# Kernel optimization log

Hardware: AMD Instinct MI355X
Metric: run time of the kernel (lower is better)

The kernel has to match this reference:

```python
import jax, jax.numpy as jnp
from jax import lax
import numpy as np

# Hyperparameters (module defaults)
MIP_K = 31
P_LO, P_HI = 0.01, 0.99
ALPHA = 0.15
MU = 10.0
PD_ITERS = 30
TAU = 0.125
SIG_PD = 0.125
THETA = 1.0
EPS = 1e-6


def _forward_grad(u):
    # forward differences, zero-padded on the far edge -> same shape as u
    dx = jnp.pad(u[..., :, 1:] - u[..., :, :-1], ((0, 0), (0, 0), (0, 0), (0, 1)))
    dy = jnp.pad(u[..., 1:, :] - u[..., :-1, :], ((0, 0), (0, 0), (0, 1), (0, 0)))
    return dx, dy


def _divergence(px, py):
    # backward-difference divergence (adjoint of forward grad)
    div_x = px - jnp.pad(px[..., :, :-1], ((0, 0), (0, 0), (0, 0), (1, 0)))
    div_y = py - jnp.pad(py[..., :-1, :], ((0, 0), (0, 0), (1, 0), (0, 0)))
    return div_x + div_y


def _max_pool(x, k):
    # stride-1 max pool with -inf padding (matches torch F.max_pool2d semantics)
    pad = k // 2
    return lax.reduce_window(
        x, -jnp.inf, lax.max,
        window_dimensions=(1, 1, k, k),
        window_strides=(1, 1, 1, 1),
        padding=((0, 0), (0, 0), (pad, pad), (pad, pad)))


def setup_inputs() -> dict:
    key = jax.random.key(0)
    Iy = jax.random.uniform(key, (16, 3, 512, 512), dtype=jnp.float32)
    return {"Iy": Iy}


def reference(Iy):
    R, G, Bc = Iy[:, 0:1], Iy[:, 1:2], Iy[:, 2:3]

    # MIP coarse depth
    Rmax = _max_pool(R, MIP_K)
    GBmax = jnp.maximum(_max_pool(G, MIP_K), _max_pool(Bc, MIP_K))
    x = jnp.abs(Rmax - GBmax) + R

    # robust per-image percentile normalization to [0,1]
    B = x.shape[0]
    flat = x.reshape(B, -1)
    lo = jnp.quantile(flat, P_LO, axis=1)[:, None, None, None]
    hi = jnp.quantile(flat, P_HI, axis=1)[:, None, None, None]
    N_hat = jnp.clip((x - lo) / (hi - lo + EPS), 0.0, 1.0)

    # fixed edge weights from grad(N_hat), sigma = per-image median grad magnitude
    dxh, dyh = _forward_grad(N_hat)
    grad_mag = jnp.sqrt(dxh * dxh + dyh * dyh + EPS)
    sigma = jnp.maximum(
        jnp.quantile(grad_mag.reshape(B, -1), 0.5, axis=1), EPS)[:, None, None, None]
    Wx = 1.0 + MU * jnp.exp(-jnp.abs(dxh) / sigma)
    Wy = 1.0 + MU * jnp.exp(-jnp.abs(dyh) / sigma)

    # Chambolle-Pock primal-dual iterations for weighted TV-L2
    def step(carry, _):
        u, u_bar, px, py = carry
        dx, dy = _forward_grad(u_bar)
        px = jnp.clip(px + SIG_PD * dx, -ALPHA * Wx, ALPHA * Wx)
        py = jnp.clip(py + SIG_PD * dy, -ALPHA * Wy, ALPHA * Wy)
        v = u + TAU * _divergence(px, py)
        u_new = (v + TAU * N_hat) / (1.0 + TAU)
        u_bar = u_new + THETA * (u_new - u)
        return (u_new, u_bar, px, py), None

    z = jnp.zeros_like(N_hat)
    (u, _, _, _), _ = lax.scan(step, (N_hat, N_hat, z, z), None, length=PD_ITERS)
    return jnp.clip(u, 0.0, 1.0)
```

## Files before the change

kernel.cpp:

```cpp
#include <hip/hip_runtime.h>
#include <math.h>

#define B_ 16
#define W_ 512
#define H_ 512
#define S_ (W_*H_)
#define ALPHA_ 0.15f
#define MU_ 10.0f
#define TAU_ 0.125f
#define SIG_ 0.125f
#define EPS_ 1e-6f
#define INV1PT_ (1.0f/(1.0f+TAU_))
#define NBINS 4096
#define BINSCALE 2048.0f
#define BINW (1.0f/2048.0f)

__global__ __launch_bounds__(256) void hmax_kernel(const float* __restrict__ Iy,
                                                   float* __restrict__ Rh,
                                                   float* __restrict__ GBh){
  __shared__ float bufA[2][544], bufB[2][544];
  int t = threadIdx.x;
  int b = blockIdx.x >> 9;
  int i = blockIdx.x & 511;
  const float* rowR = Iy + (size_t)b*3*S_ + (size_t)i*W_;
  const float* rowG = rowR + S_;
  const float* rowB = rowR + 2*S_;
  if (t < 128){
    int o4 = (t + 4)*4;
    float4 r = *(const float4*)&rowR[o4-16];
    float4 g = *(const float4*)&rowG[o4-16];
    float4 bb = *(const float4*)&rowB[o4-16];
    *(float4*)&bufA[0][o4] = r;
    *(float4*)&bufA[1][o4] = make_float4(fmaxf(g.x,bb.x), fmaxf(g.y,bb.y),
                                         fmaxf(g.z,bb.z), fmaxf(g.w,bb.w));
  } else if (t < 160){
    int e = t - 128;
    int p = (e < 16) ? e : (512 + e);
    bufA[0][p] = -1e30f;
    bufA[1][p] = -1e30f;
  }
  __syncthreads();
  float (*src)[544] = bufA; float (*dst)[544] = bufB;
  const int ds[5] = {1, 2, 4, 8, 15};
  #pragma unroll
  for (int sstep = 0; sstep < 5; ++sstep){
    int d = ds[sstep];
    for (int p = t; p < 544; p += 256){
      int q = min(p + d, 543);
      dst[0][p] = fmaxf(src[0][p], src[0][q]);
      dst[1][p] = fmaxf(src[1][p], src[1][q]);
    }
    __syncthreads();
    float (*tmp)[544] = src; src = dst; dst = tmp;
  }
  size_t o = (size_t)b*S_ + (size_t)i*W_;
  for (int p = t; p < 512; p += 256){
    Rh[o+p]  = src[0][p+1];
    GBh[o+p] = src[1][p+1];
  }
}

__global__ __launch_bounds__(256) void vscan_fwd_kernel(const float* __restrict__ Rh,
                                                        const float* __restrict__ GBh,
                                                        float* __restrict__ Rf,
                                                        float* __restrict__ Gf){
  int gid = blockIdx.x*256 + threadIdx.x;
  int col = gid & 8191;
  int c   = gid >> 13;
  int b = col >> 9, j = col & 511;
  int i0 = c*31;
  size_t base = (size_t)b*S_ + j;
  float rR = -1e30f, rG = -1e30f;
  if (c <= 15){
    for (int k = 0; k < 31; ++k){
      size_t o = base + (size_t)(i0+k)*W_;
      rR = fmaxf(rR, Rh[o]); rG = fmaxf(rG, GBh[o]);
      Rf[o] = rR; Gf[o] = rG;
    }
  } else {
    for (int k = 0; k < 16; ++k){
      size_t o = base + (size_t)(i0+k)*W_;
      rR = fmaxf(rR, Rh[o]); rG = fmaxf(rG, GBh[o]);
      Rf[o] = rR; Gf[o] = rG;
    }
  }
}

__global__ __launch_bounds__(256) void vscan_bwd_kernel(const float* __restrict__ Rh,
                                                        const float* __restrict__ GBh,
                                                        const float* __restrict__ Rf,
                                                        const float* __restrict__ Gf,
                                                        const float* __restrict__ Iy,
                                                        float* __restrict__ xo,
                                                        unsigned int* __restrict__ hist){
  __shared__ unsigned int h[NBINS];
  int t = threadIdx.x;
  for (int p = t; p < NBINS; p += 256) h[p] = 0u;
  __syncthreads();
  int gid = blockIdx.x*256 + t;
  int col = gid & 8191;
  int c   = gid >> 13;
  int b = col >> 9, j = col & 511;
  int half = j >> 8;
  int i0 = c*31;
  size_t base = (size_t)b*S_ + j;
  const float* IyR = Iy + (size_t)b*3*S_ + j;
  float lR = -1e30f, lG = -1e30f;

  #define BWD_BODY(I, BI)                                          \
    { int i_ = (I);                                                \
      size_t o64 = base + (size_t)i_*W_;                           \
      lR = fmaxf(lR, Rh[o64]); lG = fmaxf(lG, GBh[o64]);           \
      int o_ = i_ + 15;                                            \
      size_t ob = base + (size_t)(BI)*W_;                          \
      float mR = fmaxf(lR, Rf[ob]);                                \
      float mG = fmaxf(lG, Gf[ob]);                                \
      float xv = fabsf(mR - mG) + IyR[(size_t)o_*W_];              \
      xo[base + (size_t)o_*W_] = xv;                               \
      int bin = (int)(xv*BINSCALE);                                \
      bin = min(max(bin, 0), NBINS-1);                             \
      atomicAdd(&h[bin], 1u); }

  if (c <= 14){
    for (int k = 30; k >= 0; --k) BWD_BODY(i0+k, i0+k+30)
  } else if (c == 15){
    for (int k = 30; k >= 0; --k) BWD_BODY(i0+k, min(i0+k+30, H_-1))
  } else {
    for (int i = H_-1; i >= i0; --i){
      size_t o64 = base + (size_t)i*W_;
      lR = fmaxf(lR, Rh[o64]); lG = fmaxf(lG, GBh[o64]);
      int o = i + 15;
      if (o < H_){
        size_t ob = base + (size_t)(H_-1)*W_;
        float mR = fmaxf(lR, Rf[ob]);
        float mG = fmaxf(lG, Gf[ob]);
        float xv = fabsf(mR - mG) + IyR[(size_t)o*W_];
        xo[base + (size_t)o*W_] = xv;
        int bin = (int)(xv*BINSCALE);
        bin = min(max(bin, 0), NBINS-1);
        atomicAdd(&h[bin], 1u);
      }
    }
  }
  if (c == 0){
    for (int o = 0; o < 15; ++o){
      size_t ob = base + (size_t)(o+15)*W_;
      float mR = Rf[ob], mG = Gf[ob];
      float xv = fabsf(mR - mG) + IyR[(size_t)o*W_];
      xo[base + (size_t)o*W_] = xv;
      int bin = (int)(xv*BINSCALE);
      bin = min(max(bin, 0), NBINS-1);
      atomicAdd(&h[bin], 1u);
    }
  }
  __syncthreads();
  unsigned int* hb = hist + (size_t)(b*34 + c*2 + half)*NBINS;
  for (int q = t; q < NBINS; q += 256) hb[q] = h[q];
}

__global__ __launch_bounds__(256) void nhat_gmhist_kernel(const float* __restrict__ xb,
                                                          const float* __restrict__ vx2,
                                                          float* __restrict__ nh,
                                                          unsigned int* __restrict__ hist){
  __shared__ unsigned int h[NBINS];
  int t = threadIdx.x;
  int b = blockIdx.x >> 4, sub = blockIdx.x & 15;
  for (int p = t; p < NBINS; p += 256) h[p] = 0u;
  __syncthreads();
  float lo = vx2[2*b], hi = vx2[2*b+1];
  float inv = 1.0f/(hi - lo + EPS_);
  const float* base = xb + (size_t)b*S_;
  float* nhb = nh + (size_t)b*S_;
  int i0 = sub*16384;
  for (int k = 0; k < 64; ++k){
    int idx = i0 + k*256 + t;
    int row = idx >> 9, col = idx & 511;
    float c = fminf(fmaxf((base[idx] - lo)*inv, 0.f), 1.f);
    float dx = 0.f, dy = 0.f;
    if (col < W_-1) dx = fminf(fmaxf((base[idx+1]  - lo)*inv, 0.f), 1.f) - c;
    if (row < H_-1) dy = fminf(fmaxf((base[idx+W_] - lo)*inv, 0.f), 1.f) - c;
    nhb[idx] = c;
    float g = sqrtf(dx*dx + dy*dy + EPS_);
    int bin = (int)(g*BINSCALE);
    bin = min(max(bin, 0), NBINS-1);
    atomicAdd(&h[bin], 1u);
  }
  __syncthreads();
  unsigned int* hb = hist + (size_t)(b*16 + sub)*NBINS;
  for (int q = t; q < NBINS; q += 256) hb[q] = h[q];
}

__global__ __launch_bounds__(256) void pick_hist_kernel(
    const unsigned int* __restrict__ hist, int nsub,
    int r0, int r1, int r2, int r3,
    int nranks, float* __restrict__ outv, int which){
  __shared__ unsigned int part[256];
  __shared__ int s_own[4], s_rem[4];
  __shared__ float s_val[4];
  int t = threadIdx.x, b = blockIdx.x;
  const unsigned int* hb = hist + (size_t)b*nsub*NBINS;
  unsigned int binc[16];
  #pragma unroll
  for (int k = 0; k < 16; ++k) binc[k] = 0u;
  for (int sub = 0; sub < nsub; ++sub){
    const unsigned int* hp = hb + (size_t)sub*NBINS + t*16;
    #pragma unroll
    for (int k = 0; k < 16; ++k) binc[k] += hp[k];
  }
  unsigned int sum = 0u;
  #pragma unroll
  for (int k = 0; k < 16; ++k) sum += binc[k];
  part[t] = sum;
  __syncthreads();
  if (t == 0){
    int rk[4] = {r0, r1, r2, r3};
    for (int ri = 0; ri < nranks; ++ri){
      int rem = rk[ri]; int own = 255;
      for (int q = 0; q < 256; ++q){
        if ((unsigned int)rem < part[q]){ own = q; break; }
        rem -= (int)part[q];
      }
      s_own[ri] = own; s_rem[ri] = rem;
    }
  }
  __syncthreads();
  for (int ri = 0; ri < nranks; ++ri){
    if (t == s_own[ri]){
      int rem = s_rem[ri]; int bin = t*16 + 15;
      #pragma unroll
      for (int q = 0; q < 16; ++q){
        if ((unsigned int)rem < binc[q]){ bin = t*16 + q; break; }
        rem -= (int)binc[q];
      }
      s_val[ri] = ((float)bin + 0.5f) * BINW;
    }
  }
  __syncthreads();
  if (t == 0){
    if (which == 0){
      outv[2*b+0] = s_val[0]*0.57f + s_val[1]*0.43f;
      outv[2*b+1] = s_val[2]*0.43f + s_val[3]*0.57f;
    } else {
      outv[b] = fmaxf(0.5f*(s_val[0] + s_val[1]), EPS_);
    }
  }
}

#define TY 64
#define TX 64
#define HY 8
#define HX 8
#define CY 48
#define CX 48
#define NBY 11
#define NBX 11
#define PSTR 68

#define AW_(d) (ALPHA_*(1.0f + MU_*__expf(-fabsf(d)*invs)))

__global__ __launch_bounds__(1024, 2) void pd_fused_kernel(
    const float* __restrict__ u_in,  const float* __restrict__ ub_in,
    const float* __restrict__ px_in, const float* __restrict__ py_in,
    float* __restrict__ u_out,  float* __restrict__ ub_out,
    float* __restrict__ px_out, float* __restrict__ py_out,
    const float* __restrict__ nh_g, const float* __restrict__ sig_arr,
    int T, int mode)
{
  __shared__ float sA[TY*PSTR], sB[TY*PSTR], sP[TY*PSTR];
  const int t = threadIdx.x;
  const int b = blockIdx.z;
  const int gi0 = blockIdx.y*CY - HY;
  const int gj0 = blockIdx.x*CX - HX;
  const float invs = 1.0f / sig_arr[b];
  const int pi = t >> 4, pj = t & 15;
  const int c0 = 4*pj;
  const int lane = t & 63;
  const size_t bb = (size_t)b*S_;
  const int gi = gi0 + pi;

  #define STAGE(dst, srcP)                                         \
    _Pragma("unroll")                                              \
    for (int k = 0; k < 4; ++k){                                   \
      int p = t + k*1024; int li = p>>6, lj = p & 63;              \
      int sgi = gi0+li, sgj = gj0+lj;                              \
      int gic_ = min(max(sgi,0),H_-1), gjc_ = min(max(sgj,0),W_-1);\
      dst[li*PSTR+lj] = srcP[bb + (size_t)gic_*W_ + gjc_]; }

  if (mode == 1){ STAGE(sA, nh_g) }
  else          { STAGE(sA, ub_in) }

  const int rD = min(pi+1,TY-1);
  const int a_o  = pi*PSTR + c0;
  const int a_up = max(pi-1,0)*PSTR + c0;
  const int a_dn = rD*PSTR + c0;

  int gic  = min(max(gi,0),H_-1);
  int gjc4 = min(max(gj0+c0,0), W_-4);
  size_t go = bb + (size_t)gic*W_ + gjc4;
  float nh_r[4], ax[4], ay[4];
  {
    int giD = min(max(min(gi+1, gi0+TY-1),0),H_-1);
    int gjR = min(max(min(gj0+c0+4, gj0+TX-1),0),W_-1);
    float4 n0 = *(const float4*)&nh_g[go];
    float4 nD = *(const float4*)&nh_g[bb + (size_t)giD*W_ + gjc4];
    float nR = nh_g[bb + (size_t)gic*W_ + gjR];
    float n0a[4] = {n0.x,n0.y,n0.z,n0.w};
    float nDa[4] = {nD.x,nD.y,nD.z,nD.w};
    #pragma unroll
    for (int c = 0; c < 4; ++c){
      nh_r[c] = n0a[c];
      int gj = gj0 + c0 + c;
      float nhR = (c<3) ? n0a[c+1] : nR;
      bool jb = (gj < 0) || (gj >= W_-1);
      ax[c] = jb ? 0.f : AW_(nhR - n0a[c]);
      ay[c] = (gi < 0 || gi >= H_-1) ? 0.f : AW_(nDa[c] - n0a[c]);
    }
  }

  float u_r[4], px_r[4], py_r[4], ub_r[4];
  if (mode == 1){
    #pragma unroll
    for (int c = 0; c < 4; ++c){
      u_r[c] = nh_r[c]; ub_r[c] = nh_r[c];
      px_r[c] = 0.f; py_r[c] = 0.f;
    }
  } else {
    float4 uv  = *(const float4*)&u_in[go];
    float4 pxv = *(const float4*)&px_in[go];
    float4 pyv = *(const float4*)&py_in[go];
    u_r[0]=uv.x;  u_r[1]=uv.y;  u_r[2]=uv.z;  u_r[3]=uv.w;
    px_r[0]=pxv.x; px_r[1]=pxv.y; px_r[2]=pxv.z; px_r[3]=pxv.w;
    py_r[0]=pyv.x; py_r[1]=pyv.y; py_r[2]=pyv.z; py_r[3]=pyv.w;
  }
  __syncthreads();
  if (mode != 1){
    float4 ubv = *(const float4*)&sA[a_o];
    ub_r[0]=ubv.x; ub_r[1]=ubv.y; ub_r[2]=ubv.z; ub_r[3]=ubv.w;
  }

  for (int s = 0; s < T; ++s){
    float* RB = (s & 1) ? sB : sA;
    float* WB = (s & 1) ? sA : sB;
    float4 dn = *(const float4*)&RB[a_dn];
    float ubR = __shfl(ub_r[0], (lane+1)&63);
    if (pj == 15) ubR = ub_r[3];
    float dna[4] = {dn.x,dn.y,dn.z,dn.w};
    #pragma unroll
    for (int c = 0; c < 4; ++c){
      float ubRn = (c<3) ? ub_r[c+1] : ubR;
      px_r[c] = fminf(fmaxf(fmaf(SIG_, ubRn-ub_r[c], px_r[c]), -ax[c]), ax[c]);
      py_r[c] = fminf(fmaxf(fmaf(SIG_, dna[c]-ub_r[c], py_r[c]), -ay[c]), ay[c]);
    }
    *(float4*)&sP[a_o] = make_float4(py_r[0],py_r[1],py_r[2],py_r[3]);
    float pxl3 = __shfl(px_r[3], (lane-1)&63);
    __syncthreads();
    float4 pu = *(const float4*)&sP[a_up];
    float pyu[4] = {pu.x,pu.y,pu.z,pu.w};
    #pragma unroll
    for (int c = 0; c < 4; ++c){
      float pxl = (c>0) ? px_r[c-1] : pxl3;
      float div = px_r[c] + py_r[c] - pxl - pyu[c];
      float un = fmaf(TAU_, div + nh_r[c], u_r[c]) * INV1PT_;
      ub_r[c] = 2.f*un - u_r[c];
      u_r[c] = un;
    }
    if (s < T-1){
      *(float4*)&WB[a_o] = make_float4(ub_r[0],ub_r[1],ub_r[2],ub_r[3]);
      __syncthreads();
    }
  }

  if (pi >= HY && pi < HY+CY && pj >= HX/4 && pj < (HX+CX)/4 && gi < H_){
    int gj = gj0 + c0;
    if (gj < W_){
      size_t g = bb + (size_t)gi*W_ + gj;
      if (mode == 2){
        *(float4*)&u_out[g] = make_float4(
          fminf(fmaxf(u_r[0],0.f),1.f), fminf(fmaxf(u_r[1],0.f),1.f),
          fminf(fmaxf(u_r[2],0.f),1.f), fminf(fmaxf(u_r[3],0.f),1.f));
      } else {
        *(float4*)&u_out[g]  = make_float4(u_r[0], u_r[1], u_r[2], u_r[3]);
        *(float4*)&ub_out[g] = make_float4(ub_r[0],ub_r[1],ub_r[2],ub_r[3]);
        *(float4*)&px_out[g] = make_float4(px_r[0],px_r[1],px_r[2],px_r[3]);
        *(float4*)&py_out[g] = make_float4(py_r[0],py_r[1],py_r[2],py_r[3]);
      }
    }
  }
}

extern "C" void kernel_launch(void* const* d_in, const int* in_sizes, int n_in,
                              void* d_out, int out_size, void* d_ws, size_t ws_size,
                              hipStream_t stream){
  const float* Iy = (const float*)d_in[0];
  float* out = (float*)d_out;
  char* ws = (char*)d_ws;
  const size_t SLOT = (size_t)B_*S_*sizeof(float);
  float* slot[8];
  for (int q = 0; q < 8; ++q) slot[q] = (float*)(ws + (size_t)q*SLOT);
  float* vx2 = (float*)(ws + (size_t)8*SLOT);
  float* sig = vx2 + 32;

  float* Rh  = slot[0];
  float* GBh = slot[1];
  float* Rf  = slot[5];
  float* Gf  = slot[6];
  float* xb  = slot[2];
  float* nh  = slot[3];
  unsigned int* hist_x  = (unsigned int*)(ws + (size_t)4*SLOT);
  unsigned int* hist_gm = (unsigned int*)(ws + (size_t)4*SLOT + 9437184);

  hmax_kernel<<<B_*H_, 256, 0, stream>>>(Iy, Rh, GBh);
  vscan_fwd_kernel<<<544, 256, 0, stream>>>(Rh, GBh, Rf, Gf);
  vscan_bwd_kernel<<<544, 256, 0, stream>>>(Rh, GBh, Rf, Gf, Iy, xb, hist_x);
  pick_hist_kernel<<<B_, 256, 0, stream>>>(hist_x, 34, 2621, 2622, 259521, 259522, 4, vx2, 0);
  nhat_gmhist_kernel<<<256, 256, 0, stream>>>(xb, vx2, nh, hist_gm);
  pick_hist_kernel<<<B_, 256, 0, stream>>>(hist_gm, 16, 131071, 131072, 0, 0, 2, sig, 1);

  float *uA = slot[1], *ubA = slot[2], *pxA = slot[5], *pyA = slot[6];
  float *uB = slot[0], *ubB = slot[4], *pxB = slot[7], *pyB = out;

  dim3 pdg(NBX, NBY, B_);
  pd_fused_kernel<<<pdg, 1024, 0, stream>>>(nh, nh, nh, nh,
                                            uA, ubA, pxA, pyA, nh, sig, 8, 1);
  pd_fused_kernel<<<pdg, 1024, 0, stream>>>(uA, ubA, pxA, pyA,
                                            uB, ubB, pxB, pyB, nh, sig, 8, 0);
  pd_fused_kernel<<<pdg, 1024, 0, stream>>>(uB, ubB, pxB, pyB,
                                            uA, ubA, pxA, pyA, nh, sig, 8, 0);
  pd_fused_kernel<<<pdg, 1024, 0, stream>>>(uA, ubA, pxA, pyA,
                                            out, slot[7], slot[7], slot[7], nh, sig, 6, 2);
}
```

Before: 380.3 us.

## Fuse vertical max-pool scans into one kernel and vectorize N_hat gradient histogram

The forward and backward vertical van Herk scans are merged into a single kernel. Each column chunk is staged in shared memory and the suffix max is built there, so the Rf/Gf prefix arrays are no longer written to and read back from global memory. The N_hat/gradient-histogram kernel now processes four pixels per thread with float4 loads and stores. The fused kernel uses about 79 KB of shared memory per block, which lowers occupancy and adds extra rereads of the next chunk's rows.

After: 345.2 us. -9.2%, faster.

```diff
diff --git a/kernel.cpp b/kernel.cpp
--- a/kernel.cpp
+++ b/kernel.cpp
@@ -60,39 +60,11 @@
   }
 }
 
-__global__ __launch_bounds__(256) void vscan_fwd_kernel(const float* __restrict__ Rh,
-                                                        const float* __restrict__ GBh,
-                                                        float* __restrict__ Rf,
-                                                        float* __restrict__ Gf){
-  int gid = blockIdx.x*256 + threadIdx.x;
-  int col = gid & 8191;
-  int c   = gid >> 13;
-  int b = col >> 9, j = col & 511;
-  int i0 = c*31;
-  size_t base = (size_t)b*S_ + j;
-  float rR = -1e30f, rG = -1e30f;
-  if (c <= 15){
-    for (int k = 0; k < 31; ++k){
-      size_t o = base + (size_t)(i0+k)*W_;
-      rR = fmaxf(rR, Rh[o]); rG = fmaxf(rG, GBh[o]);
-      Rf[o] = rR; Gf[o] = rG;
-    }
-  } else {
-    for (int k = 0; k < 16; ++k){
-      size_t o = base + (size_t)(i0+k)*W_;
-      rR = fmaxf(rR, Rh[o]); rG = fmaxf(rG, GBh[o]);
-      Rf[o] = rR; Gf[o] = rG;
-    }
-  }
-}
-
-__global__ __launch_bounds__(256) void vscan_bwd_kernel(const float* __restrict__ Rh,
-                                                        const float* __restrict__ GBh,
-                                                        const float* __restrict__ Rf,
-                                                        const float* __restrict__ Gf,
-                                                        const float* __restrict__ Iy,
-                                                        float* __restrict__ xo,
-                                                        unsigned int* __restrict__ hist){
+__global__ __launch_bounds__(256) void vscan_fused_kernel(
+    const float* __restrict__ Rh, const float* __restrict__ GBh,
+    const float* __restrict__ Iy, float* __restrict__ xo,
+    unsigned int* __restrict__ hist){
+  __shared__ float sR[31*256], sG[31*256];
   __shared__ unsigned int h[NBINS];
   int t = threadIdx.x;
   for (int p = t; p < NBINS; p += 256) h[p] = 0u;
@@ -105,53 +77,65 @@
   int i0 = c*31;
   size_t base = (size_t)b*S_ + j;
   const float* IyR = Iy + (size_t)b*3*S_ + j;
-  float lR = -1e30f, lG = -1e30f;
-
-  #define BWD_BODY(I, BI)                                          \
-    { int i_ = (I);                                                \
-      size_t o64 = base + (size_t)i_*W_;                           \
-      lR = fmaxf(lR, Rh[o64]); lG = fmaxf(lG, GBh[o64]);           \
-      int o_ = i_ + 15;                                            \
-      size_t ob = base + (size_t)(BI)*W_;                          \
-      float mR = fmaxf(lR, Rf[ob]);                                \
-      float mG = fmaxf(lG, Gf[ob]);                                \
-      float xv = fabsf(mR - mG) + IyR[(size_t)o_*W_];              \
-      xo[base + (size_t)o_*W_] = xv;                               \
-      int bin = (int)(xv*BINSCALE);                                \
-      bin = min(max(bin, 0), NBINS-1);                             \
-      atomicAdd(&h[bin], 1u); }
-
-  if (c <= 14){
-    for (int k = 30; k >= 0; --k) BWD_BODY(i0+k, i0+k+30)
-  } else if (c == 15){
-    for (int k = 30; k >= 0; --k) BWD_BODY(i0+k, min(i0+k+30, H_-1))
+
+  #define EMIT(OROW, XV)                                   \
+    { float xv_ = (XV);                                    \
+      xo[base + (size_t)(OROW)*W_] = xv_;                  \
+      int bin_ = (int)(xv_*BINSCALE);                      \
+      bin_ = min(max(bin_, 0), NBINS-1);                   \
+      atomicAdd(&h[bin_], 1u); }
+
+  if (c < 16){
+    if (c == 0){
+      float hR = -1e30f, hG = -1e30f;
+      for (int k = 0; k < 31; ++k){
+        size_t o64 = base + (size_t)k*W_;
+        float vR = Rh[o64], vG = GBh[o64];
+        sR[k*256+t] = vR; sG[k*256+t] = vG;
+        hR = fmaxf(hR, vR); hG = fmaxf(hG, vG);
+        if (k >= 15 && k <= 29){
+          int o = k - 15;
+          EMIT(o, fabsf(hR - hG) + IyR[(size_t)o*W_])
+        }
+      }
+    } else {
+      for (int k = 0; k < 31; ++k){
+        size_t o64 = base + (size_t)(i0+k)*W_;
+        sR[k*256+t] = Rh[o64]; sG[k*256+t] = GBh[o64];
+      }
+    }
+    {
+      float runR = -1e30f, runG = -1e30f;
+      for (int k = 30; k >= 0; --k){
+        runR = fmaxf(runR, sR[k*256+t]);
+        runG = fmaxf(runG, sG[k*256+t]);
+        sR[k*256+t] = runR; sG[k*256+t] = runG;
+      }
+    }
+    {
+      float mR = sR[t], mG = sG[t];
+      int o0 = i0 + 15;
+      EMIT(o0, fabsf(mR - mG) + IyR[(size_t)o0*W_])
+      float pR = -1e30f, pG = -1e30f;
+      for (int k = 1; k <= 30; ++k){
+        int ri = i0 + 30 + k;
+        if (ri < H_){
+          size_t o64 = base + (size_t)ri*W_;
+          pR = fmaxf(pR, Rh[o64]); pG = fmaxf(pG, GBh[o64]);
+        }
+        float mRk = fmaxf(sR[k*256+t], pR);
+        float mGk = fmaxf(sG[k*256+t], pG);
+        int ok = i0 + k + 15;
+        EMIT(ok, fabsf(mRk - mGk) + IyR[(size_t)ok*W_])
+      }
+    }
   } else {
-    for (int i = H_-1; i >= i0; --i){
+    float runR = -1e30f, runG = -1e30f;
+    for (int i = H_-1; i >= 496; --i){
       size_t o64 = base + (size_t)i*W_;
-      lR = fmaxf(lR, Rh[o64]); lG = fmaxf(lG, GBh[o64]);
-      int o = i + 15;
-      if (o < H_){
-        size_t ob = base + (size_t)(H_-1)*W_;
-        float mR = fmaxf(lR, Rf[ob]);
-        float mG = fmaxf(lG, Gf[ob]);
-        float xv = fabsf(mR - mG) + IyR[(size_t)o*W_];
-        xo[base + (size_t)o*W_] = xv;
-        int bin = (int)(xv*BINSCALE);
-        bin = min(max(bin, 0), NBINS-1);
-        atomicAdd(&h[bin], 1u);
-      }
-    }
-  }
-  if (c == 0){
-    for (int o = 0; o < 15; ++o){
-      size_t ob = base + (size_t)(o+15)*W_;
-      float mR = Rf[ob], mG = Gf[ob];
-      float xv = fabsf(mR - mG) + IyR[(size_t)o*W_];
-      xo[base + (size_t)o*W_] = xv;
-      int bin = (int)(xv*BINSCALE);
-      bin = min(max(bin, 0), NBINS-1);
-      atomicAdd(&h[bin], 1u);
-    }
+      runR = fmaxf(runR, Rh[o64]); runG = fmaxf(runG, GBh[o64]);
+    }
+    EMIT(H_-1, fabsf(runR - runG) + IyR[(size_t)(H_-1)*W_])
   }
   __syncthreads();
   unsigned int* hb = hist + (size_t)(b*34 + c*2 + half)*NBINS;
@@ -172,18 +156,32 @@
   const float* base = xb + (size_t)b*S_;
   float* nhb = nh + (size_t)b*S_;
   int i0 = sub*16384;
-  for (int k = 0; k < 64; ++k){
-    int idx = i0 + k*256 + t;
-    int row = idx >> 9, col = idx & 511;
-    float c = fminf(fmaxf((base[idx] - lo)*inv, 0.f), 1.f);
-    float dx = 0.f, dy = 0.f;
-    if (col < W_-1) dx = fminf(fmaxf((base[idx+1]  - lo)*inv, 0.f), 1.f) - c;
-    if (row < H_-1) dy = fminf(fmaxf((base[idx+W_] - lo)*inv, 0.f), 1.f) - c;
-    nhb[idx] = c;
-    float g = sqrtf(dx*dx + dy*dy + EPS_);
-    int bin = (int)(g*BINSCALE);
-    bin = min(max(bin, 0), NBINS-1);
-    atomicAdd(&h[bin], 1u);
+  #define NCLP(V) fminf(fmaxf(((V) - lo)*inv, 0.f), 1.f)
+  for (int k = 0; k < 16; ++k){
+    int idx = i0 + (k*256 + t)*4;
+    int row = idx >> 9, col0 = idx & 511;
+    float4 v = *(const float4*)&base[idx];
+    float c0 = NCLP(v.x), c1 = NCLP(v.y), c2 = NCLP(v.z), c3 = NCLP(v.w);
+    float cn = (col0 < 508) ? NCLP(base[idx+4]) : 0.f;
+    float d0x = c1 - c0, d1x = c2 - c1, d2x = c3 - c2;
+    float d3x = (col0 < 508) ? (cn - c3) : 0.f;
+    float d0y = 0.f, d1y = 0.f, d2y = 0.f, d3y = 0.f;
+    if (row < H_-1){
+      float4 w = *(const float4*)&base[idx+W_];
+      d0y = NCLP(w.x) - c0; d1y = NCLP(w.y) - c1;
+      d2y = NCLP(w.z) - c2; d3y = NCLP(w.w) - c3;
+    }
+    *(float4*)&nhb[idx] = make_float4(c0, c1, c2, c3);
+    float g0 = sqrtf(d0x*d0x + d0y*d0y + EPS_);
+    float g1 = sqrtf(d1x*d1x + d1y*d1y + EPS_);
+    float g2 = sqrtf(d2x*d2x + d2y*d2y + EPS_);
+    float g3 = sqrtf(d3x*d3x + d3y*d3y + EPS_);
+    int b0 = min(max((int)(g0*BINSCALE), 0), NBINS-1);
+    int b1 = min(max((int)(g1*BINSCALE), 0), NBINS-1);
+    int b2 = min(max((int)(g2*BINSCALE), 0), NBINS-1);
+    int b3 = min(max((int)(g3*BINSCALE), 0), NBINS-1);
+    atomicAdd(&h[b0], 1u); atomicAdd(&h[b1], 1u);
+    atomicAdd(&h[b2], 1u); atomicAdd(&h[b3], 1u);
   }
   __syncthreads();
   unsigned int* hb = hist + (size_t)(b*16 + sub)*NBINS;
@@ -402,16 +400,13 @@
 
   float* Rh  = slot[0];
   float* GBh = slot[1];
-  float* Rf  = slot[5];
-  float* Gf  = slot[6];
   float* xb  = slot[2];
   float* nh  = slot[3];
   unsigned int* hist_x  = (unsigned int*)(ws + (size_t)4*SLOT);
   unsigned int* hist_gm = (unsigned int*)(ws + (size_t)4*SLOT + 9437184);
 
   hmax_kernel<<<B_*H_, 256, 0, stream>>>(Iy, Rh, GBh);
-  vscan_fwd_kernel<<<544, 256, 0, stream>>>(Rh, GBh, Rf, Gf);
-  vscan_bwd_kernel<<<544, 256, 0, stream>>>(Rh, GBh, Rf, Gf, Iy, xb, hist_x);
+  vscan_fused_kernel<<<544, 256, 0, stream>>>(Rh, GBh, Iy, xb, hist_x);
   pick_hist_kernel<<<B_, 256, 0, stream>>>(hist_x, 34, 2621, 2622, 259521, 259522, 4, vx2, 0);
   nhat_gmhist_kernel<<<256, 256, 0, stream>>>(xb, vx2, nh, hist_gm);
   pick_hist_kernel<<<B_, 256, 0, stream>>>(hist_gm, 16, 131071, 131072, 0, 0, 2, sig, 1);
```
